# Optimization experiments

Hardware: AMD Instinct MI355X
Metric: run time of the kernel (lower is better)

## Reference

```python
import jax, jax.numpy as jnp
import numpy as np

SEGMENT_LENGTHS = (2048, 4096, 8192)
DILATION_RATES = (1, 2, 4)
NUM_HEADS = 12
EMBED_DIM = 768
B, N = 2, 8192


def setup_inputs() -> dict:
    key = jax.random.key(0)
    ks = jax.random.split(key, 11)
    E = EMBED_DIM
    return {
        "query": jax.random.normal(ks[0], (B, N, E), jnp.float32),
        "key": jax.random.normal(ks[1], (B, N, E), jnp.float32),
        "value": jax.random.normal(ks[2], (B, N, E), jnp.float32),
        "Wq": jax.random.normal(ks[3], (E, E), jnp.float32) * (E ** -0.5),
        "bq": jax.random.normal(ks[4], (E,), jnp.float32) * 0.02,
        "Wk": jax.random.normal(ks[5], (E, E), jnp.float32) * (E ** -0.5),
        "bk": jax.random.normal(ks[6], (E,), jnp.float32) * 0.02,
        "Wv": jax.random.normal(ks[7], (E, E), jnp.float32) * (E ** -0.5),
        "bv": jax.random.normal(ks[8], (E,), jnp.float32) * 0.02,
        "Wo": jax.random.normal(ks[9], (E, E), jnp.float32) * (E ** -0.5),
        "bo": jax.random.normal(ks[10], (E,), jnp.float32) * 0.02,
    }


def _dilated_attention(q, k, v):
    # q, k, v: [b, n, h, d]
    b, n, h, d = q.shape
    num_groups = len(DILATION_RATES)
    g = h // num_groups  # heads per dilation group
    scale = float(1.0 / np.sqrt(d))  # xformers default softmax scale
    out = jnp.zeros_like(q)
    for i, (r, s) in enumerate(zip(DILATION_RATES, SEGMENT_LENGTHS)):
        off = i % r
        hmin, hmax = i * g, (i + 1) * g
        nseg = n // s
        # gather: [b, nseg, s/r, g, d]
        qg = q.reshape(b, nseg, s, h, d)[:, :, off::r, hmin:hmax, :]
        kg = k.reshape(b, nseg, s, h, d)[:, :, off::r, hmin:hmax, :]
        vg = v.reshape(b, nseg, s, h, d)[:, :, off::r, hmin:hmax, :]
        scores = jnp.einsum("bnqhd,bnkhd->bnhqk", qg, kg) * scale
        attn = jax.nn.softmax(scores, axis=-1)
        x = jnp.einsum("bnhqk,bnkhd->bnqhd", attn, vg)
        out = (
            out.reshape(b, nseg, s, h, d)
            .at[:, :, off::r, hmin:hmax, :]
            .add(x)
            .reshape(b, n, h, d)
        )
    # faithful to original: normalize by sum over the sequence dimension
    return out / jnp.sum(out, axis=1, keepdims=True)


def reference(query, key, value, Wq, bq, Wk, bk, Wv, bv, Wo, bo):
    b, n, e = query.shape
    h = NUM_HEADS
    d = e // h
    q = (query @ Wq.T + bq).reshape(b, n, h, d)
    k = (key @ Wk.T + bk).reshape(b, n, h, d)
    v = (value @ Wv.T + bv).reshape(b, n, h, d)
    x = _dilated_attention(q, k, v)
    x = x.reshape(b, n, e)
    return x @ Wo.T + bo
```

## Files before the change

kernel.cpp:

```cpp
#include <hip/hip_runtime.h>
#include <hip/hip_bf16.h>
#include <cmath>
#include <cstdint>

#define B_ 2
#define N_ 8192
#define H_ 12
#define D_ 64
#define E_ 768
#define M_ (B_*N_)

typedef __attribute__((ext_vector_type(8))) short short8;
typedef __attribute__((ext_vector_type(4))) short short4v;
typedef __attribute__((ext_vector_type(4))) float float4v;

__device__ inline short f2b(float f) {
  union { float f; unsigned u; } x; x.f = f;
  unsigned r = (x.u + 0x7fffu + ((x.u >> 16) & 1u)) >> 16;
  return (short)r;
}
__device__ inline float b2f(short s) {
  union { unsigned u; float f; } x; x.u = ((unsigned)(unsigned short)s) << 16;
  return x.f;
}
__device__ inline void split2(float f, short& h, short& l) {
  h = f2b(f);
  l = f2b(f - b2f(h));
}

#define MFMA(a, b, c) __builtin_amdgcn_mfma_f32_16x16x32_bf16((a), (b), (c), 0, 0, 0)

__global__ __launch_bounds__(256) void split_kernel(const float* __restrict__ src,
    short* __restrict__ hi, short* __restrict__ lo, int count4)
{
  int i = blockIdx.x * 256 + threadIdx.x;
  if (i >= count4) return;
  float4v t = ((const float4v*)src)[i];
  short4v h4, l4; short hh, ll;
  split2(t.x, hh, ll); h4.x = hh; l4.x = ll;
  split2(t.y, hh, ll); h4.y = hh; l4.y = ll;
  split2(t.z, hh, ll); h4.z = hh; l4.z = ll;
  split2(t.w, hh, ll); h4.w = hh; l4.w = ll;
  ((short4v*)hi)[i] = h4;
  ((short4v*)lo)[i] = l4;
}

template<bool A_PAIR, bool OUT_PAIR>
__global__ __launch_bounds__(256) void gemm_xwT(const void* __restrict__ Ap,
    const short* __restrict__ Alo, const short* __restrict__ Wh,
    const short* __restrict__ Wl, const float* __restrict__ bias,
    void* __restrict__ OutH, short* __restrict__ OutL)
{
  __shared__ short Ash[128 * 40], Asl[128 * 40];
  __shared__ short Wsh[128 * 40], Wsl[128 * 40];
  const int tid = threadIdx.x;
  const int m0 = blockIdx.y * 128;
  const int n0 = blockIdx.x * 128;
  const int w = tid >> 6, lane = tid & 63, quad = lane >> 4, l16 = lane & 15;
  const int wr = w >> 1, wc = w & 1;

  float4v acc[4][4];
#pragma unroll
  for (int a = 0; a < 4; ++a)
#pragma unroll
    for (int c = 0; c < 4; ++c) acc[a][c] = (float4v)0.0f;

  for (int kt = 0; kt < 24; ++kt) {
    const int k0 = kt * 32;
#pragma unroll
    for (int p = 0; p < 4; ++p) {
      int idx = tid + p * 256;
      int row = idx >> 3, c4 = (idx & 7) * 4;
      short4v avh, avl;
      if constexpr (A_PAIR) {
        avh = *(const short4v*)((const short*)Ap + (size_t)(m0 + row) * E_ + k0 + c4);
        avl = *(const short4v*)(Alo + (size_t)(m0 + row) * E_ + k0 + c4);
      } else {
        float4v t = *(const float4v*)((const float*)Ap + (size_t)(m0 + row) * E_ + k0 + c4);
        short hh, ll;
        split2(t.x, hh, ll); avh.x = hh; avl.x = ll;
        split2(t.y, hh, ll); avh.y = hh; avl.y = ll;
        split2(t.z, hh, ll); avh.z = hh; avl.z = ll;
        split2(t.w, hh, ll); avh.w = hh; avl.w = ll;
      }
      *(short4v*)&Ash[row * 40 + c4] = avh;
      *(short4v*)&Asl[row * 40 + c4] = avl;
      *(short4v*)&Wsh[row * 40 + c4] = *(const short4v*)(Wh + (size_t)(n0 + row) * E_ + k0 + c4);
      *(short4v*)&Wsl[row * 40 + c4] = *(const short4v*)(Wl + (size_t)(n0 + row) * E_ + k0 + c4);
    }
    __syncthreads();

    short8 afh[4], afl[4], bfh[4], bfl[4];
#pragma unroll
    for (int rt = 0; rt < 4; ++rt) {
      afh[rt] = *(const short8*)&Ash[(wr * 64 + rt * 16 + l16) * 40 + quad * 8];
      afl[rt] = *(const short8*)&Asl[(wr * 64 + rt * 16 + l16) * 40 + quad * 8];
    }
#pragma unroll
    for (int ct = 0; ct < 4; ++ct) {
      bfh[ct] = *(const short8*)&Wsh[(wc * 64 + ct * 16 + l16) * 40 + quad * 8];
      bfl[ct] = *(const short8*)&Wsl[(wc * 64 + ct * 16 + l16) * 40 + quad * 8];
    }
#pragma unroll
    for (int rt = 0; rt < 4; ++rt)
#pragma unroll
      for (int ct = 0; ct < 4; ++ct) {
        float4v a = acc[rt][ct];
        a = MFMA(afh[rt], bfh[ct], a);
        a = MFMA(afh[rt], bfl[ct], a);
        a = MFMA(afl[rt], bfh[ct], a);
        acc[rt][ct] = a;
      }
    __syncthreads();
  }

#pragma unroll
  for (int ct = 0; ct < 4; ++ct) {
    int n = n0 + wc * 64 + ct * 16 + l16;
    float bv = bias[n];
#pragma unroll
    for (int rt = 0; rt < 4; ++rt) {
#pragma unroll
      for (int i = 0; i < 4; ++i) {
        int m = m0 + wr * 64 + rt * 16 + quad * 4 + i;
        float v = acc[rt][ct][i] + bv;
        if constexpr (OUT_PAIR) {
          short hh, ll; split2(v, hh, ll);
          ((short*)OutH)[(size_t)m * E_ + n] = hh;
          OutL[(size_t)m * E_ + n] = ll;
        } else {
          ((float*)OutH)[(size_t)m * E_ + n] = v;
        }
      }
    }
  }
}

__device__ __host__ inline int hoff_of(int g, int hg) {
  return g == 0 ? hg * 8192 : (g == 1 ? 32768 + hg * 4096 : 49152 + hg * 2048);
}

__global__ __launch_bounds__(256) void transpose_v(const short* __restrict__ vh,
    const short* __restrict__ vl, short* __restrict__ vgh, short* __restrict__ vgl)
{
  __shared__ short Lh[64 * 68], Ll[64 * 68];
  int bid = blockIdx.x;
  int b = 0;
  if (bid >= 896) { b = 1; bid -= 896; }
  int g, hg, tile;
  if (bid < 512)      { g = 0; hg = bid >> 7; tile = bid & 127; }
  else if (bid < 768) { g = 1; hg = (bid - 512) >> 6; tile = (bid - 512) & 63; }
  else                { g = 2; hg = (bid - 768) >> 5; tile = (bid - 768) & 31; }
  const int h = g * 4 + hg, r = 1 << g, off = g;
  const int ext = 8192 >> g;
  const int jj0 = tile * 64, seg = jj0 >> 11, j0 = jj0 & 2047;
  const int n0 = seg * (2048 << g) + off + j0 * r;
  const int tid = threadIdx.x;

#pragma unroll
  for (int p = 0; p < 2; ++p) {
    int c = tid + p * 256;
    int jr = c >> 3, c8 = (c & 7) * 8;
    size_t gsrc = ((size_t)(b * N_ + n0 + jr * r) * H_ + h) * D_ + c8;
    *(short8*)&Lh[jr * 68 + c8] = *(const short8*)(vh + gsrc);
    *(short8*)&Ll[jr * 68 + c8] = *(const short8*)(vl + gsrc);
  }
  __syncthreads();
  size_t basebh = ((size_t)b * 57344 + hoff_of(g, hg)) * 64;
#pragma unroll
  for (int p = 0; p < 2; ++p) {
    int c = tid + p * 256;
    int dd = c >> 3, jc = (c & 7) * 8;
    short8 oh, ol;
#pragma unroll
    for (int u = 0; u < 8; ++u) {
      oh[u] = Lh[(jc + u) * 68 + dd];
      ol[u] = Ll[(jc + u) * 68 + dd];
    }
    size_t gdst = basebh + (size_t)dd * ext + jj0 + jc;
    *(short8*)(vgh + gdst) = oh;
    *(short8*)(vgl + gdst) = ol;
  }
}

__global__ __launch_bounds__(256) void attn_kernel(
    const short* __restrict__ qh, const short* __restrict__ ql,
    const short* __restrict__ kh, const short* __restrict__ kl,
    const short* __restrict__ vgh, const short* __restrict__ vgl,
    float* __restrict__ attn_out, float* __restrict__ sums)
{
  __shared__ short Ksh[32 * 72], Ksl[32 * 72];
  __shared__ short Vth[64 * 40], Vtl[64 * 40];
  __shared__ short Psh[4][32 * 40], Psl[4][32 * 40];

  int bid = blockIdx.x;
  int g, t;
  if (bid < 512)      { g = 0; t = bid; }
  else if (bid < 768) { g = 1; t = bid - 512; }
  else                { g = 2; t = bid - 768; }
  const int qtile = t & 15; t >>= 4;
  const int hg = t & 3; t >>= 2;
  const int nseg = 4 >> g;
  const int seg = t & (nseg - 1);
  const int b = t / nseg;
  const int r = 1 << g;
  const int off = g;
  const int h = g * 4 + hg;
  const int segbase = seg * (2048 << g);
  const int ext = 8192 >> g;

  const int tid = threadIdx.x;
  const int w = tid >> 6, lane = tid & 63, quad = lane >> 4, l16 = lane & 15;

  const size_t vbase = ((size_t)b * 57344 + hoff_of(g, hg)) * 64 + (size_t)seg * 2048;

  short8 qfh[2][2], qfl[2][2];
#pragma unroll
  for (int qt = 0; qt < 2; ++qt) {
    int j = qtile * 128 + w * 32 + qt * 16 + l16;
    int pos = segbase + off + j * r;
    size_t base = ((size_t)(b * N_ + pos) * H_ + h) * D_;
#pragma unroll
    for (int ks = 0; ks < 2; ++ks) {
      qfh[qt][ks] = *(const short8*)(qh + base + ks * 32 + quad * 8);
      qfl[qt][ks] = *(const short8*)(ql + base + ks * 32 + quad * 8);
    }
  }

  float4v o[4][2];
  float mrow[2], lrow[2];
#pragma unroll
  for (int dt = 0; dt < 4; ++dt)
#pragma unroll
    for (int qt = 0; qt < 2; ++qt) o[dt][qt] = (float4v)0.0f;
  mrow[0] = mrow[1] = -INFINITY;
  lrow[0] = lrow[1] = 0.f;

  for (int kt = 0; kt < 64; ++kt) {
    {
      int row = tid & 31, c8 = (tid >> 5) * 8;
      int posk = segbase + off + (kt * 32 + row) * r;
      size_t gb = ((size_t)(b * N_ + posk) * H_ + h) * D_ + c8;
      *(short8*)&Ksh[row * 72 + c8] = *(const short8*)(kh + gb);
      *(short8*)&Ksl[row * 72 + c8] = *(const short8*)(kl + gb);
      int dd = tid >> 2, kvc = (tid & 3) * 8;
      size_t vb = vbase + (size_t)dd * ext + kt * 32 + kvc;
      *(short8*)&Vth[dd * 40 + kvc] = *(const short8*)(vgh + vb);
      *(short8*)&Vtl[dd * 40 + kvc] = *(const short8*)(vgl + vb);
    }
    __syncthreads();

    float4v sc[2][2];
#pragma unroll
    for (int kvt = 0; kvt < 2; ++kvt) {
      const int kb = (kvt * 16 + l16) * 72 + quad * 8;
      short8 ah0 = *(const short8*)&Ksh[kb];
      short8 ah1 = *(const short8*)&Ksh[kb + 32];
      short8 al0 = *(const short8*)&Ksl[kb];
      short8 al1 = *(const short8*)&Ksl[kb + 32];
#pragma unroll
      for (int qt = 0; qt < 2; ++qt) {
        float4v a = (float4v)0.0f;
        a = MFMA(ah0, qfh[qt][0], a); a = MFMA(ah1, qfh[qt][1], a);
        a = MFMA(ah0, qfl[qt][0], a); a = MFMA(ah1, qfl[qt][1], a);
        a = MFMA(al0, qfh[qt][0], a); a = MFMA(al1, qfh[qt][1], a);
        sc[qt][kvt] = a * 0.125f;
      }
    }

#pragma unroll
    for (int qt = 0; qt < 2; ++qt) {
      float mx = sc[qt][0][0];
#pragma unroll
      for (int kvt = 0; kvt < 2; ++kvt)
#pragma unroll
        for (int i = 0; i < 4; ++i) mx = fmaxf(mx, sc[qt][kvt][i]);
      mx = fmaxf(mx, __shfl_xor(mx, 16, 64));
      mx = fmaxf(mx, __shfl_xor(mx, 32, 64));
      float mnew = fmaxf(mrow[qt], mx);
      float alpha = __expf(mrow[qt] - mnew);
      mrow[qt] = mnew;
      float rs = 0.f;
#pragma unroll
      for (int kvt = 0; kvt < 2; ++kvt)
#pragma unroll
        for (int i = 0; i < 4; ++i) {
          float p = __expf(sc[qt][kvt][i] - mnew);
          sc[qt][kvt][i] = p;
          rs += p;
        }
      rs += __shfl_xor(rs, 16, 64);
      rs += __shfl_xor(rs, 32, 64);
      lrow[qt] = lrow[qt] * alpha + rs;
#pragma unroll
      for (int dt = 0; dt < 4; ++dt) o[dt][qt] *= alpha;

#pragma unroll
      for (int kvt = 0; kvt < 2; ++kvt)
#pragma unroll
        for (int c = 0; c < 2; ++c) {
          short h0, l0, h1, l1;
          split2(sc[qt][kvt][2 * c], h0, l0);
          split2(sc[qt][kvt][2 * c + 1], h1, l1);
          int ad = (qt * 16 + l16) * 40 + kvt * 16 + quad * 4 + 2 * c;
          *(unsigned*)&Psh[w][ad] = (unsigned)(unsigned short)h0 | ((unsigned)(unsigned short)h1 << 16);
          *(unsigned*)&Psl[w][ad] = (unsigned)(unsigned short)l0 | ((unsigned)(unsigned short)l1 << 16);
        }
    }

    short8 pfh[2], pfl[2];
#pragma unroll
    for (int qt = 0; qt < 2; ++qt) {
      pfh[qt] = *(const short8*)&Psh[w][(qt * 16 + l16) * 40 + quad * 8];
      pfl[qt] = *(const short8*)&Psl[w][(qt * 16 + l16) * 40 + quad * 8];
    }
#pragma unroll
    for (int dt = 0; dt < 4; ++dt) {
      short8 vfh = *(const short8*)&Vth[(dt * 16 + l16) * 40 + quad * 8];
      short8 vfl = *(const short8*)&Vtl[(dt * 16 + l16) * 40 + quad * 8];
#pragma unroll
      for (int qt = 0; qt < 2; ++qt) {
        float4v a = o[dt][qt];
        a = MFMA(vfh, pfh[qt], a);
        a = MFMA(vfh, pfl[qt], a);
        a = MFMA(vfl, pfh[qt], a);
        o[dt][qt] = a;
      }
    }
    __syncthreads();
  }

  float4v sacc[4];
#pragma unroll
  for (int dt = 0; dt < 4; ++dt) sacc[dt] = (float4v)0.0f;
#pragma unroll
  for (int qt = 0; qt < 2; ++qt) {
    float inv_l = 1.0f / lrow[qt];
    int j = qtile * 128 + w * 32 + qt * 16 + l16;
    int pos = segbase + off + j * r;
    float* dst = attn_out + ((size_t)(b * N_ + pos) * H_ + h) * D_;
#pragma unroll
    for (int dt = 0; dt < 4; ++dt) {
      float4v v = o[dt][qt] * inv_l;
      *(float4v*)(dst + dt * 16 + quad * 4) = v;
      sacc[dt] += v;
    }
  }
#pragma unroll
  for (int dt = 0; dt < 4; ++dt) {
#pragma unroll
    for (int i = 0; i < 4; ++i) {
      float x = sacc[dt][i];
      x += __shfl_xor(x, 1, 64);
      x += __shfl_xor(x, 2, 64);
      x += __shfl_xor(x, 4, 64);
      x += __shfl_xor(x, 8, 64);
      if (l16 == 0)
        atomicAdd(&sums[(size_t)b * E_ + h * D_ + dt * 16 + quad * 4 + i], x);
    }
  }
}

__global__ __launch_bounds__(256) void normalize_kernel(const float* __restrict__ attn,
    const float* __restrict__ sums, short* __restrict__ xnh, short* __restrict__ xnl)
{
  size_t e4 = ((size_t)blockIdx.x * 256 + threadIdx.x) * 4;
  int e = (int)(e4 % E_);
  int nn = (int)((e4 / E_) % N_);
  int b = (int)(e4 / ((size_t)E_ * N_));
  int g = e >> 8;
  int r = 1 << g;
  int off = g & (r - 1);
  short4v oh, ol;
  if ((nn & (r - 1)) == off) {
    float4v a = *(const float4v*)(attn + e4);
    const float* sp = sums + (size_t)b * E_ + e;
    short hh, ll;
    split2(a.x / sp[0], hh, ll); oh.x = hh; ol.x = ll;
    split2(a.y / sp[1], hh, ll); oh.y = hh; ol.y = ll;
    split2(a.z / sp[2], hh, ll); oh.z = hh; ol.z = ll;
    split2(a.w / sp[3], hh, ll); oh.w = hh; ol.w = ll;
  } else {
    oh = (short4v)(short)0;
    ol = (short4v)(short)0;
  }
  *(short4v*)&xnh[e4] = oh;
  *(short4v*)&xnl[e4] = ol;
}

extern "C" void kernel_launch(void* const* d_in, const int* in_sizes, int n_in,
                              void* d_out, int out_size, void* d_ws, size_t ws_size,
                              hipStream_t stream)
{
  const float* query = (const float*)d_in[0];
  const float* key_  = (const float*)d_in[1];
  const float* value = (const float*)d_in[2];
  const float* Wq = (const float*)d_in[3];
  const float* bq = (const float*)d_in[4];
  const float* Wk = (const float*)d_in[5];
  const float* bk = (const float*)d_in[6];
  const float* Wv = (const float*)d_in[7];
  const float* bv = (const float*)d_in[8];
  const float* Wo = (const float*)d_in[9];
  const float* bo = (const float*)d_in[10];

  char* ws = (char*)d_ws;
  const size_t szbf = (size_t)M_ * E_ * 2;
  const size_t szvg = (size_t)2 * 57344 * 64 * 2;
  const size_t szw  = (size_t)E_ * E_ * 2;
  short* qh_ = (short*)(ws);
  short* ql_ = (short*)(ws + 1 * szbf);
  short* kh_ = (short*)(ws + 2 * szbf);
  short* kl_ = (short*)(ws + 3 * szbf);
  short* vh_ = (short*)(ws + 4 * szbf);
  short* vl_ = (short*)(ws + 5 * szbf);
  short* vgh = (short*)(ws + 6 * szbf);
  short* vgl = (short*)(ws + 6 * szbf + szvg);
  short* wsp = (short*)(ws + 6 * szbf + 2 * szvg);
  short* wqh = wsp + 0 * (szw / 2), *wql = wsp + 1 * (szw / 2);
  short* wkh = wsp + 2 * (szw / 2), *wkl = wsp + 3 * (szw / 2);
  short* wvh = wsp + 4 * (szw / 2), *wvl = wsp + 5 * (szw / 2);
  short* woh = wsp + 6 * (szw / 2), *wol = wsp + 7 * (szw / 2);
  float* sums = (float*)(ws + 6 * szbf + 2 * szvg + 8 * szw);
  float* attn = (float*)(ws + 4 * szbf);
  short* xnh = kh_;
  short* xnl = kl_;

  hipMemsetAsync(sums, 0, (size_t)B_ * E_ * sizeof(float), stream);

  const int wc4 = E_ * E_ / 4;
  split_kernel<<<(wc4 + 255) / 256, 256, 0, stream>>>(Wq, wqh, wql, wc4);
  split_kernel<<<(wc4 + 255) / 256, 256, 0, stream>>>(Wk, wkh, wkl, wc4);
  split_kernel<<<(wc4 + 255) / 256, 256, 0, stream>>>(Wv, wvh, wvl, wc4);
  split_kernel<<<(wc4 + 255) / 256, 256, 0, stream>>>(Wo, woh, wol, wc4);

  dim3 gg(6, 128), gb(256);
  gemm_xwT<false, true><<<gg, gb, 0, stream>>>(query, nullptr, wqh, wql, bq, qh_, ql_);
  gemm_xwT<false, true><<<gg, gb, 0, stream>>>(key_,  nullptr, wkh, wkl, bk, kh_, kl_);
  gemm_xwT<false, true><<<gg, gb, 0, stream>>>(value, nullptr, wvh, wvl, bv, vh_, vl_);
  transpose_v<<<1792, 256, 0, stream>>>(vh_, vl_, vgh, vgl);
  attn_kernel<<<896, 256, 0, stream>>>(qh_, ql_, kh_, kl_, vgh, vgl, attn, sums);
  normalize_kernel<<<12288, 256, 0, stream>>>(attn, sums, xnh, xnl);
  gemm_xwT<true, false><<<gg, gb, 0, stream>>>(xnh, xnl, woh, wol, bo, d_out, nullptr);
}
```

Before: 948.7 us.

## Fuse normalization into output GEMM, async W loads, lazy softmax rescale

Removes the separate normalize kernel. The output projection GEMM now reads the fp32 attention output directly, scales it by precomputed reciprocal column sums, and splits it into bf16 hi/lo pairs on the fly. The attention kernel zero-fills the non-strided positions that normalize used to write. Weight tiles are loaded with global_load_lds into an XOR-swizzled unpadded LDS layout. The softmax rescale is skipped when no row max grows, and the lo parts of the P and A splits use truncation instead of round-to-nearest, which slightly changes numerics.

New measurement: 886.5 us. 6.6% less time.

```diff
diff --git a/kernel.cpp b/kernel.cpp
--- a/kernel.cpp
+++ b/kernel.cpp
@@ -13,6 +13,7 @@
 typedef __attribute__((ext_vector_type(8))) short short8;
 typedef __attribute__((ext_vector_type(4))) short short4v;
 typedef __attribute__((ext_vector_type(4))) float float4v;
+typedef __attribute__((ext_vector_type(2))) unsigned uint2v;
 
 __device__ inline short f2b(float f) {
   union { float f; unsigned u; } x; x.f = f;
@@ -27,8 +28,21 @@
   h = f2b(f);
   l = f2b(f - b2f(h));
 }
+__device__ inline void split_rn1(float f, unsigned& hi16, float& lo) {
+  unsigned u = __float_as_uint(f);
+  unsigned r = u + 0x7fffu + ((u >> 16) & 1u);
+  hi16 = r >> 16;
+  lo = f - __uint_as_float(hi16 << 16);
+}
+__device__ inline unsigned pack_trunc(float a, float b) {
+  return (__float_as_uint(b) & 0xffff0000u) | (__float_as_uint(a) >> 16);
+}
 
 #define MFMA(a, b, c) __builtin_amdgcn_mfma_f32_16x16x32_bf16((a), (b), (c), 0, 0, 0)
+
+#define GLOAD_LDS16(g, l) \
+  __builtin_amdgcn_global_load_lds((const __attribute__((address_space(1))) void*)(g), \
+      (__attribute__((address_space(3))) void*)(l), 16, 0, 0)
 
 __global__ __launch_bounds__(256) void split_kernel(const float* __restrict__ src,
     short* __restrict__ hi, short* __restrict__ lo, int count4)
@@ -45,19 +59,27 @@
   ((short4v*)lo)[i] = l4;
 }
 
-template<bool A_PAIR, bool OUT_PAIR>
-__global__ __launch_bounds__(256) void gemm_xwT(const void* __restrict__ Ap,
-    const short* __restrict__ Alo, const short* __restrict__ Wh,
+__global__ __launch_bounds__(256) void inv_kernel(const float* __restrict__ sums,
+    float* __restrict__ inv)
+{
+  int i = blockIdx.x * 256 + threadIdx.x;
+  if (i < B_ * E_) inv[i] = 1.0f / sums[i];
+}
+
+template<int AMODE, bool OUT_PAIR>
+__global__ __launch_bounds__(256) void gemm_xwT(const float* __restrict__ Ap,
+    const float* __restrict__ inv, const short* __restrict__ Wh,
     const short* __restrict__ Wl, const float* __restrict__ bias,
     void* __restrict__ OutH, short* __restrict__ OutL)
 {
   __shared__ short Ash[128 * 40], Asl[128 * 40];
-  __shared__ short Wsh[128 * 40], Wsl[128 * 40];
+  __shared__ short Wsh[128 * 32], Wsl[128 * 32];
   const int tid = threadIdx.x;
   const int m0 = blockIdx.y * 128;
   const int n0 = blockIdx.x * 128;
   const int w = tid >> 6, lane = tid & 63, quad = lane >> 4, l16 = lane & 15;
   const int wr = w >> 1, wc = w & 1;
+  const int cq = (l16 >> 1) & 3;
 
   float4v acc[4][4];
 #pragma unroll
@@ -67,26 +89,32 @@
 
   for (int kt = 0; kt < 24; ++kt) {
     const int k0 = kt * 32;
+#pragma unroll
+    for (int i = 0; i < 2; ++i) {
+      int slot = w * 128 + i * 64 + lane;
+      int row = slot >> 2, cs = slot & 3;
+      int cl = cs ^ ((row >> 1) & 3);
+      size_t go = (size_t)(n0 + row) * E_ + k0 + cl * 8;
+      GLOAD_LDS16(Wh + go, &Wsh[slot * 8]);
+      GLOAD_LDS16(Wl + go, &Wsl[slot * 8]);
+    }
 #pragma unroll
     for (int p = 0; p < 4; ++p) {
       int idx = tid + p * 256;
       int row = idx >> 3, c4 = (idx & 7) * 4;
-      short4v avh, avl;
-      if constexpr (A_PAIR) {
-        avh = *(const short4v*)((const short*)Ap + (size_t)(m0 + row) * E_ + k0 + c4);
-        avl = *(const short4v*)(Alo + (size_t)(m0 + row) * E_ + k0 + c4);
-      } else {
-        float4v t = *(const float4v*)((const float*)Ap + (size_t)(m0 + row) * E_ + k0 + c4);
-        short hh, ll;
-        split2(t.x, hh, ll); avh.x = hh; avl.x = ll;
-        split2(t.y, hh, ll); avh.y = hh; avl.y = ll;
-        split2(t.z, hh, ll); avh.z = hh; avl.z = ll;
-        split2(t.w, hh, ll); avh.w = hh; avl.w = ll;
-      }
-      *(short4v*)&Ash[row * 40 + c4] = avh;
-      *(short4v*)&Asl[row * 40 + c4] = avl;
-      *(short4v*)&Wsh[row * 40 + c4] = *(const short4v*)(Wh + (size_t)(n0 + row) * E_ + k0 + c4);
-      *(short4v*)&Wsl[row * 40 + c4] = *(const short4v*)(Wl + (size_t)(n0 + row) * E_ + k0 + c4);
+      float4v t = *(const float4v*)(Ap + (size_t)(m0 + row) * E_ + k0 + c4);
+      if constexpr (AMODE == 1) {
+        float4v iv = *(const float4v*)(inv + (m0 >> 13) * E_ + k0 + c4);
+        t *= iv;
+      }
+      unsigned h0, h1, h2, h3; float l0, l1, l2, l3;
+      split_rn1(t.x, h0, l0); split_rn1(t.y, h1, l1);
+      split_rn1(t.z, h2, l2); split_rn1(t.w, h3, l3);
+      uint2v hp, lp;
+      hp.x = h0 | (h1 << 16); hp.y = h2 | (h3 << 16);
+      lp.x = pack_trunc(l0, l1); lp.y = pack_trunc(l2, l3);
+      *(uint2v*)&Ash[row * 40 + c4] = hp;
+      *(uint2v*)&Asl[row * 40 + c4] = lp;
     }
     __syncthreads();
 
@@ -98,8 +126,9 @@
     }
 #pragma unroll
     for (int ct = 0; ct < 4; ++ct) {
-      bfh[ct] = *(const short8*)&Wsh[(wc * 64 + ct * 16 + l16) * 40 + quad * 8];
-      bfl[ct] = *(const short8*)&Wsl[(wc * 64 + ct * 16 + l16) * 40 + quad * 8];
+      int wrow = (wc * 64 + ct * 16 + l16) * 32 + (quad ^ cq) * 8;
+      bfh[ct] = *(const short8*)&Wsh[wrow];
+      bfl[ct] = *(const short8*)&Wsl[wrow];
     }
 #pragma unroll
     for (int rt = 0; rt < 4; ++rt)
@@ -214,6 +243,20 @@
 
   const size_t vbase = ((size_t)b * 57344 + hoff_of(g, hg)) * 64 + (size_t)seg * 2048;
 
+  if (g > 0) {
+#pragma unroll
+    for (int res0 = 1; res0 < 4; ++res0) {
+      if (res0 >= r) break;
+      int res = (off + res0) & (r - 1);
+      for (int c = 0; c < 8; ++c) {
+        int idx = tid + c * 256;
+        int jl = idx >> 4, d0 = (idx & 15) * 4;
+        int pos = segbase + res + (qtile * 128 + jl) * r;
+        *(float4v*)(attn_out + ((size_t)(b * N_ + pos) * H_ + h) * D_ + d0) = (float4v)0.f;
+      }
+    }
+  }
+
   short8 qfh[2][2], qfl[2][2];
 #pragma unroll
   for (int qt = 0; qt < 2; ++qt) {
@@ -238,7 +281,7 @@
 
   for (int kt = 0; kt < 64; ++kt) {
     {
-      int row = tid & 31, c8 = (tid >> 5) * 8;
+      int row = tid >> 3, c8 = (tid & 7) * 8;
       int posk = segbase + off + (kt * 32 + row) * r;
       size_t gb = ((size_t)(b * N_ + posk) * H_ + h) * D_ + c8;
       *(short8*)&Ksh[row * 72 + c8] = *(const short8*)(kh + gb);
@@ -277,34 +320,38 @@
         for (int i = 0; i < 4; ++i) mx = fmaxf(mx, sc[qt][kvt][i]);
       mx = fmaxf(mx, __shfl_xor(mx, 16, 64));
       mx = fmaxf(mx, __shfl_xor(mx, 32, 64));
-      float mnew = fmaxf(mrow[qt], mx);
-      float alpha = __expf(mrow[qt] - mnew);
-      mrow[qt] = mnew;
+      if (__any(mx > mrow[qt])) {
+        float mnew = fmaxf(mrow[qt], mx);
+        float alpha = __expf(mrow[qt] - mnew);
+        mrow[qt] = mnew;
+        lrow[qt] *= alpha;
+#pragma unroll
+        for (int dt = 0; dt < 4; ++dt) o[dt][qt] *= alpha;
+      }
       float rs = 0.f;
 #pragma unroll
       for (int kvt = 0; kvt < 2; ++kvt)
 #pragma unroll
         for (int i = 0; i < 4; ++i) {
-          float p = __expf(sc[qt][kvt][i] - mnew);
+          float p = __expf(sc[qt][kvt][i] - mrow[qt]);
           sc[qt][kvt][i] = p;
           rs += p;
         }
       rs += __shfl_xor(rs, 16, 64);
       rs += __shfl_xor(rs, 32, 64);
-      lrow[qt] = lrow[qt] * alpha + rs;
-#pragma unroll
-      for (int dt = 0; dt < 4; ++dt) o[dt][qt] *= alpha;
+      lrow[qt] += rs;
 
 #pragma unroll
       for (int kvt = 0; kvt < 2; ++kvt)
 #pragma unroll
         for (int c = 0; c < 2; ++c) {
-          short h0, l0, h1, l1;
-          split2(sc[qt][kvt][2 * c], h0, l0);
-          split2(sc[qt][kvt][2 * c + 1], h1, l1);
+          float pa = sc[qt][kvt][2 * c], pb = sc[qt][kvt][2 * c + 1];
+          unsigned ua = __float_as_uint(pa), ub = __float_as_uint(pb);
+          float la = pa - __uint_as_float(ua & 0xffff0000u);
+          float lb = pb - __uint_as_float(ub & 0xffff0000u);
           int ad = (qt * 16 + l16) * 40 + kvt * 16 + quad * 4 + 2 * c;
-          *(unsigned*)&Psh[w][ad] = (unsigned)(unsigned short)h0 | ((unsigned)(unsigned short)h1 << 16);
-          *(unsigned*)&Psl[w][ad] = (unsigned)(unsigned short)l0 | ((unsigned)(unsigned short)l1 << 16);
+          *(unsigned*)&Psh[w][ad] = (ub & 0xffff0000u) | (ua >> 16);
+          *(unsigned*)&Psl[w][ad] = pack_trunc(la, lb);
         }
     }
 
@@ -359,33 +406,6 @@
         atomicAdd(&sums[(size_t)b * E_ + h * D_ + dt * 16 + quad * 4 + i], x);
     }
   }
-}
-
-__global__ __launch_bounds__(256) void normalize_kernel(const float* __restrict__ attn,
-    const float* __restrict__ sums, short* __restrict__ xnh, short* __restrict__ xnl)
-{
-  size_t e4 = ((size_t)blockIdx.x * 256 + threadIdx.x) * 4;
-  int e = (int)(e4 % E_);
-  int nn = (int)((e4 / E_) % N_);
-  int b = (int)(e4 / ((size_t)E_ * N_));
-  int g = e >> 8;
-  int r = 1 << g;
-  int off = g & (r - 1);
-  short4v oh, ol;
-  if ((nn & (r - 1)) == off) {
-    float4v a = *(const float4v*)(attn + e4);
-    const float* sp = sums + (size_t)b * E_ + e;
-    short hh, ll;
-    split2(a.x / sp[0], hh, ll); oh.x = hh; ol.x = ll;
-    split2(a.y / sp[1], hh, ll); oh.y = hh; ol.y = ll;
-    split2(a.z / sp[2], hh, ll); oh.z = hh; ol.z = ll;
-    split2(a.w / sp[3], hh, ll); oh.w = hh; ol.w = ll;
-  } else {
-    oh = (short4v)(short)0;
-    ol = (short4v)(short)0;
-  }
-  *(short4v*)&xnh[e4] = oh;
-  *(short4v*)&xnl[e4] = ol;
 }
 
 extern "C" void kernel_launch(void* const* d_in, const int* in_sizes, int n_in,
@@ -423,8 +443,7 @@
   short* woh = wsp + 6 * (szw / 2), *wol = wsp + 7 * (szw / 2);
   float* sums = (float*)(ws + 6 * szbf + 2 * szvg + 8 * szw);
   float* attn = (float*)(ws + 4 * szbf);
-  short* xnh = kh_;
-  short* xnl = kl_;
+  float* inv  = (float*)qh_;
 
   hipMemsetAsync(sums, 0, (size_t)B_ * E_ * sizeof(float), stream);
 
@@ -435,11 +454,11 @@
   split_kernel<<<(wc4 + 255) / 256, 256, 0, stream>>>(Wo, woh, wol, wc4);
 
   dim3 gg(6, 128), gb(256);
-  gemm_xwT<false, true><<<gg, gb, 0, stream>>>(query, nullptr, wqh, wql, bq, qh_, ql_);
-  gemm_xwT<false, true><<<gg, gb, 0, stream>>>(key_,  nullptr, wkh, wkl, bk, kh_, kl_);
-  gemm_xwT<false, true><<<gg, gb, 0, stream>>>(value, nullptr, wvh, wvl, bv, vh_, vl_);
+  gemm_xwT<0, true><<<gg, gb, 0, stream>>>(query, nullptr, wqh, wql, bq, qh_, ql_);
+  gemm_xwT<0, true><<<gg, gb, 0, stream>>>(key_,  nullptr, wkh, wkl, bk, kh_, kl_);
+  gemm_xwT<0, true><<<gg, gb, 0, stream>>>(value, nullptr, wvh, wvl, bv, vh_, vl_);
   transpose_v<<<1792, 256, 0, stream>>>(vh_, vl_, vgh, vgl);
   attn_kernel<<<896, 256, 0, stream>>>(qh_, ql_, kh_, kl_, vgh, vgl, attn, sums);
-  normalize_kernel<<<12288, 256, 0, stream>>>(attn, sums, xnh, xnl);
-  gemm_xwT<true, false><<<gg, gb, 0, stream>>>(xnh, xnl, woh, wol, bo, d_out, nullptr);
-}
+  inv_kernel<<<6, 256, 0, stream>>>(sums, inv);
+  gemm_xwT<1, false><<<gg, gb, 0, stream>>>(attn, inv, woh, wol, bo, d_out, nullptr);
+}
```
